# Kernel tuning notes

Hardware: AMD Instinct MI355X
Metric: run time of the kernel (lower is better)

The kernel has to match this reference:

```python
import jax, jax.numpy as jnp
import numpy as np

COMMITMENT_COST = 0.25


def setup_inputs() -> dict:
    key = jax.random.key(0)
    k1, k2 = jax.random.split(key)
    inputs = jax.random.normal(k1, (32, 64, 32, 32), dtype=jnp.float32)  # (B, C, H, W)
    embed = jax.random.normal(k2, (64, 1024), dtype=jnp.float32)          # (embedding_dim, num_embeddings)
    return {"inputs": inputs, "embed": embed}


def reference(inputs, embed):
    # Eval-mode forward (EMA buffer updates are training-only side effects).
    B, C, H, W = inputs.shape
    K = embed.shape[1]
    flat = inputs.transpose(0, 2, 3, 1).reshape(-1, C)  # (N, C)
    N = flat.shape[0]

    distances = (jnp.sum(flat * flat, axis=1, keepdims=True)
                 + jnp.sum(embed * embed, axis=0)
                 - 2.0 * flat @ embed)
    encoding_indices = jnp.argmin(distances, axis=1)  # (N,)

    # Gather instead of one-hot @ embed.T (same math, no N x K one-hot)
    quantized = embed.T[encoding_indices]  # (N, C)

    e_latent_loss = jnp.mean((jax.lax.stop_gradient(quantized) - flat) ** 2)
    loss = COMMITMENT_COST * e_latent_loss

    # straight-through estimator
    quantized_st = flat + jax.lax.stop_gradient(quantized - flat)
    quantized_out = quantized_st.reshape(B, H, W, C).transpose(0, 3, 1, 2)

    # avg_probs via scatter-add counts (== mean of one-hot encodings)
    counts = jnp.zeros((K,), dtype=flat.dtype).at[encoding_indices].add(1.0)
    avg_probs = counts / N
    perplexity = jnp.exp(-jnp.sum(avg_probs * jnp.log(avg_probs + 1e-10)))

    return quantized_out, loss, encoding_indices, perplexity
```

## Files before the change

kernel.cpp:

```cpp
#include <hip/hip_runtime.h>

#define N_PIX  32768
#define C_DIM  64
#define K_EMB  1024
#define HW     1024
#define P_TILE 8

#define OUT_Q_OFF    0
#define OUT_LOSS_OFF 2097152
#define OUT_IDX_OFF  2097153
#define OUT_PERP_OFF 2129921


__device__ __forceinline__ unsigned long long pack_score(float d, int k) {
    unsigned int u = __float_as_uint(d);
    u = (u & 0x80000000u) ? ~u : (u | 0x80000000u);
    return ((unsigned long long)u << 32) | (unsigned int)k;
}

__global__ __launch_bounds__(256, 4) void k_main(
    const float* __restrict__ inp, const float* __restrict__ embed,
    unsigned int* __restrict__ counts, float* __restrict__ lossAcc,
    float* __restrict__ out_q, float* __restrict__ out_idx) {
    __shared__ float x_lds[C_DIM * P_TILE];
    __shared__ unsigned long long red[4][P_TILE];
    __shared__ int ksel[P_TILE];
    __shared__ float lred[2];

    const int tid = threadIdx.x;
    const int n0  = blockIdx.x * P_TILE;
    const int b   = n0 >> 10;
    const int hw0 = n0 & 1023;
    const float* __restrict__ xu = inp + b * (C_DIM * HW) + hw0;

    if (tid < 128) {
        const int c  = tid >> 1;
        const int p4 = (tid & 1) * 4;
        *reinterpret_cast<float4*>(&x_lds[c * P_TILE + p4]) =
            *reinterpret_cast<const float4*>(xu + c * HW + p4);
    }
    __syncthreads();

    const int k0 = tid * 4;
    const float4* __restrict__ eb =
        reinterpret_cast<const float4*>(embed) + (k0 >> 2);

    float4 a0 = {0,0,0,0}, a1 = {0,0,0,0}, a2 = {0,0,0,0}, a3 = {0,0,0,0};
    float4 a4 = {0,0,0,0}, a5 = {0,0,0,0}, a6 = {0,0,0,0}, a7 = {0,0,0,0};
    float4 ee = {0,0,0,0};

#define FMA_P(i, xv, E) \
    a##i.x = fmaf((xv), E.x, a##i.x); \
    a##i.y = fmaf((xv), E.y, a##i.y); \
    a##i.z = fmaf((xv), E.z, a##i.z); \
    a##i.w = fmaf((xv), E.w, a##i.w);

#define BODY(E, c) { \
    const float4 xq0 = *reinterpret_cast<const float4*>(&x_lds[(c) * P_TILE + 0]); \
    const float4 xq1 = *reinterpret_cast<const float4*>(&x_lds[(c) * P_TILE + 4]); \
    ee.x = fmaf(E.x, E.x, ee.x); ee.y = fmaf(E.y, E.y, ee.y); \
    ee.z = fmaf(E.z, E.z, ee.z); ee.w = fmaf(E.w, E.w, ee.w); \
    FMA_P(0, xq0.x, E) FMA_P(1, xq0.y, E) FMA_P(2, xq0.z, E) FMA_P(3, xq0.w, E) \
    FMA_P(4, xq1.x, E) FMA_P(5, xq1.y, E) FMA_P(6, xq1.z, E) FMA_P(7, xq1.w, E) }

    float4 E0 = eb[0 * 256], E1 = eb[1 * 256], E2 = eb[2 * 256], E3 = eb[3 * 256];
#pragma unroll 1
    for (int c = 0; c < C_DIM; c += 4) {
        const int cn = (c + 4 < C_DIM) ? (c + 4) : c;
        float4 N0 = eb[(cn + 0) * 256];
        float4 N1 = eb[(cn + 1) * 256];
        float4 N2 = eb[(cn + 2) * 256];
        float4 N3 = eb[(cn + 3) * 256];
        BODY(E0, c + 0)
        BODY(E1, c + 1)
        BODY(E2, c + 2)
        BODY(E3, c + 3)
        E0 = N0; E1 = N1; E2 = N2; E3 = N3;
    }
#undef BODY
#undef FMA_P

    const int wv = tid >> 6, ln = tid & 63;
#define RED_P(i) { \
        const float s0 = fmaf(-2.f, a##i.x, ee.x); \
        const float s1 = fmaf(-2.f, a##i.y, ee.y); \
        const float s2 = fmaf(-2.f, a##i.z, ee.z); \
        const float s3 = fmaf(-2.f, a##i.w, ee.w); \
        unsigned long long m = pack_score(s0, k0), t; \
        t = pack_score(s1, k0 + 1); if (t < m) m = t; \
        t = pack_score(s2, k0 + 2); if (t < m) m = t; \
        t = pack_score(s3, k0 + 3); if (t < m) m = t; \
        for (int off = 32; off > 0; off >>= 1) { \
            unsigned long long o = __shfl_down(m, off, 64); \
            if (o < m) m = o; \
        } \
        if (ln == 0) red[wv][i] = m; }
    RED_P(0) RED_P(1) RED_P(2) RED_P(3)
    RED_P(4) RED_P(5) RED_P(6) RED_P(7)
#undef RED_P

    __syncthreads();
    if (tid < P_TILE) {
        unsigned long long m = red[0][tid];
        if (red[1][tid] < m) m = red[1][tid];
        if (red[2][tid] < m) m = red[2][tid];
        if (red[3][tid] < m) m = red[3][tid];
        const int k = (int)(unsigned int)(m & 0xFFFFFFFFull);
        ksel[tid] = k;
        out_idx[n0 + tid] = (float)k;
        atomicAdd(counts + k, 1u);
    }
    __syncthreads();

    if (tid < 128) {
        const int c  = tid >> 1;
        const int pb = (tid & 1) * 4;
        float ls = 0.f;
        float4 qv;
        float* qvp = &qv.x;
#pragma unroll
        for (int j = 0; j < 4; ++j) {
            const int k = ksel[pb + j];
            const float q  = embed[c * K_EMB + k];
            const float xv = x_lds[c * P_TILE + pb + j];
            const float d  = q - xv;
            ls = fmaf(d, d, ls);
            qvp[j] = q;
        }
        *reinterpret_cast<float4*>(out_q + b * (C_DIM * HW) + c * HW + hw0 + pb) = qv;
        for (int off = 32; off > 0; off >>= 1) ls += __shfl_down(ls, off, 64);
        if (ln == 0) lred[wv] = ls;
    }
    __syncthreads();
    if (tid == 0) atomicAdd(lossAcc, lred[0] + lred[1]);
}

__global__ __launch_bounds__(1024) void k_scalar(
    const unsigned int* __restrict__ counts, const float* __restrict__ lossAcc,
    float* __restrict__ out_loss, float* __restrict__ out_perp) {
    __shared__ float red[16];
    const int tid = threadIdx.x;
    float p = (float)counts[tid] * (1.0f / (float)N_PIX);
    float t = p * logf(p + 1e-10f);
    for (int off = 32; off > 0; off >>= 1) t += __shfl_down(t, off, 64);
    if ((tid & 63) == 0) red[tid >> 6] = t;
    __syncthreads();
    if (tid == 0) {
        float s = 0.f;
#pragma unroll
        for (int i = 0; i < 16; ++i) s += red[i];
        *out_perp = expf(-s);
        *out_loss = 0.25f * (*lossAcc) * (1.0f / (float)(N_PIX * C_DIM));
    }
}

extern "C" void kernel_launch(void* const* d_in, const int* in_sizes, int n_in,
                              void* d_out, int out_size, void* d_ws, size_t ws_size,
                              hipStream_t stream) {
    const float* inp   = (const float*)d_in[0];
    const float* embed = (const float*)d_in[1];
    float* out = (float*)d_out;

    char* ws = (char*)d_ws;
    unsigned int* counts  = (unsigned int*)(ws + 0);
    float*        lossAcc = (float*)(ws + 4096);

    hipMemsetAsync(ws, 0, 4096 + 16, stream);

    k_main<<<dim3(N_PIX / P_TILE), dim3(256), 0, stream>>>(
        inp, embed, counts, lossAcc, out + OUT_Q_OFF, out + OUT_IDX_OFF);
    k_scalar<<<dim3(1), dim3(1024), 0, stream>>>(counts, lossAcc,
        out + OUT_LOSS_OFF, out + OUT_PERP_OFF);
}
```

Baseline: 144.6 us.

## Compute distances with split-bf16 MFMA and exact fp32 top-2 rescoring

Replaces the scalar fp32 FMA distance loop with bf16 MFMA 32x32x16 instructions. Both the codebook and the inputs are split into three bf16 parts to approximate fp32 precision. A prep kernel precomputes the split codebook and the codebook norms, and the main kernel processes 64 pixels per block while tracking the top-2 candidates per pixel. The two candidates are rescored in exact fp32 so the argmin stays correct. The loss is computed algebraically from ||x||^2 plus the best distance, and the memset is replaced by zeroing device globals in the prep kernel. This trades some extra prep work, precision risk from the reduced-term split, and lower occupancy for much higher matrix throughput.

```diff
diff --git a/kernel.cpp b/kernel.cpp
--- a/kernel.cpp
+++ b/kernel.cpp
@@ -4,145 +4,257 @@
 #define C_DIM  64
 #define K_EMB  1024
 #define HW     1024
-#define P_TILE 8
+#define PIXB   64
 
 #define OUT_Q_OFF    0
 #define OUT_LOSS_OFF 2097152
 #define OUT_IDX_OFF  2097153
 #define OUT_PERP_OFF 2129921
 
-
+typedef __attribute__((ext_vector_type(8)))  __bf16 bf16x8;
+typedef __attribute__((ext_vector_type(16))) float  f32x16;
+
+__device__ unsigned short g_esplit[3 * K_EMB * C_DIM];
+__device__ float          g_ee[K_EMB];
+__device__ unsigned int   g_counts[K_EMB];
+__device__ float          g_lossAcc;
+
+__device__ __forceinline__ unsigned short f2bf(float f) {
+    unsigned u = __float_as_uint(f);
+    unsigned r = u + 0x7FFFu + ((u >> 16) & 1u);
+    return (unsigned short)(r >> 16);
+}
+__device__ __forceinline__ float bf2f(unsigned short b) {
+    return __uint_as_float(((unsigned)b) << 16);
+}
 __device__ __forceinline__ unsigned long long pack_score(float d, int k) {
     unsigned int u = __float_as_uint(d);
     u = (u & 0x80000000u) ? ~u : (u | 0x80000000u);
     return ((unsigned long long)u << 32) | (unsigned int)k;
 }
-
-__global__ __launch_bounds__(256, 4) void k_main(
+__device__ __forceinline__ uint4 pack8(const unsigned short* v) {
+    uint4 u;
+    u.x = (unsigned)v[0] | ((unsigned)v[1] << 16);
+    u.y = (unsigned)v[2] | ((unsigned)v[3] << 16);
+    u.z = (unsigned)v[4] | ((unsigned)v[5] << 16);
+    u.w = (unsigned)v[6] | ((unsigned)v[7] << 16);
+    return u;
+}
+__device__ __forceinline__ unsigned long long shfl_xor32_u64(unsigned long long v) {
+    unsigned lo = (unsigned)v, hi = (unsigned)(v >> 32);
+    lo = __shfl_xor(lo, 32, 64);
+    hi = __shfl_xor(hi, 32, 64);
+    return ((unsigned long long)hi << 32) | lo;
+}
+#define UPD2(P1, P2, MM) { \
+    if ((MM) < P1) { P2 = P1; P1 = (MM); } else if ((MM) < P2) P2 = (MM); }
+#define MRG2(P1, P2, O1, O2) { \
+    unsigned long long _lo = (O1) < P1 ? (O1) : P1; \
+    unsigned long long _hi = (O1) < P1 ? P1 : (O1); \
+    unsigned long long _m2 = (O2) < P2 ? (O2) : P2; \
+    P1 = _lo; P2 = _hi < _m2 ? _hi : _m2; }
+
+__global__ void k_prep(const float* __restrict__ embed) {
+    const int code = blockIdx.x * 64 + threadIdx.x;
+    if (code == 0) g_lossAcc = 0.f;
+    g_counts[code] = 0u;
+    const int tile = code >> 5, c32 = code & 31;
+    float ee = 0.f;
+#pragma unroll 8
+    for (int c = 0; c < C_DIM; ++c) {
+        const float x = embed[c * K_EMB + code];
+        ee = fmaf(x, x, ee);
+        const unsigned short b1 = f2bf(x);
+        const float r1 = x - bf2f(b1);
+        const unsigned short b2 = f2bf(r1);
+        const float r2 = r1 - bf2f(b2);
+        const unsigned short b3 = f2bf(r2);
+        const int s = c >> 4, hh = (c >> 3) & 1, e = c & 7;
+        const int rest = ((((tile * 4 + s) * 2 + hh) * 32) + c32) * 8 + e;
+        g_esplit[rest          ] = b1;
+        g_esplit[rest +  65536 ] = b2;
+        g_esplit[rest + 131072 ] = b3;
+    }
+    g_ee[code] = ee;
+}
+
+__global__ __launch_bounds__(256, 2) void k_main(
     const float* __restrict__ inp, const float* __restrict__ embed,
-    unsigned int* __restrict__ counts, float* __restrict__ lossAcc,
     float* __restrict__ out_q, float* __restrict__ out_idx) {
-    __shared__ float x_lds[C_DIM * P_TILE];
-    __shared__ unsigned long long red[4][P_TILE];
-    __shared__ int ksel[P_TILE];
-    __shared__ float lred[2];
+
+    __shared__ float x_raw[C_DIM * PIXB];
+    __shared__ uint4 xfrag[3 * 4 * 2 * PIXB];
+    __shared__ unsigned long long red1[4][PIXB];
+    __shared__ unsigned long long red2[4][PIXB];
+    __shared__ int   ksel[PIXB];
+    __shared__ float lred[4];
+    __shared__ float bdist;
 
     const int tid = threadIdx.x;
-    const int n0  = blockIdx.x * P_TILE;
+    const int n0  = blockIdx.x * PIXB;
     const int b   = n0 >> 10;
     const int hw0 = n0 & 1023;
-    const float* __restrict__ xu = inp + b * (C_DIM * HW) + hw0;
-
-    if (tid < 128) {
-        const int c  = tid >> 1;
-        const int p4 = (tid & 1) * 4;
-        *reinterpret_cast<float4*>(&x_lds[c * P_TILE + p4]) =
-            *reinterpret_cast<const float4*>(xu + c * HW + p4);
-    }
-    __syncthreads();
-
-    const int k0 = tid * 4;
-    const float4* __restrict__ eb =
-        reinterpret_cast<const float4*>(embed) + (k0 >> 2);
-
-    float4 a0 = {0,0,0,0}, a1 = {0,0,0,0}, a2 = {0,0,0,0}, a3 = {0,0,0,0};
-    float4 a4 = {0,0,0,0}, a5 = {0,0,0,0}, a6 = {0,0,0,0}, a7 = {0,0,0,0};
-    float4 ee = {0,0,0,0};
-
-#define FMA_P(i, xv, E) \
-    a##i.x = fmaf((xv), E.x, a##i.x); \
-    a##i.y = fmaf((xv), E.y, a##i.y); \
-    a##i.z = fmaf((xv), E.z, a##i.z); \
-    a##i.w = fmaf((xv), E.w, a##i.w);
-
-#define BODY(E, c) { \
-    const float4 xq0 = *reinterpret_cast<const float4*>(&x_lds[(c) * P_TILE + 0]); \
-    const float4 xq1 = *reinterpret_cast<const float4*>(&x_lds[(c) * P_TILE + 4]); \
-    ee.x = fmaf(E.x, E.x, ee.x); ee.y = fmaf(E.y, E.y, ee.y); \
-    ee.z = fmaf(E.z, E.z, ee.z); ee.w = fmaf(E.w, E.w, ee.w); \
-    FMA_P(0, xq0.x, E) FMA_P(1, xq0.y, E) FMA_P(2, xq0.z, E) FMA_P(3, xq0.w, E) \
-    FMA_P(4, xq1.x, E) FMA_P(5, xq1.y, E) FMA_P(6, xq1.z, E) FMA_P(7, xq1.w, E) }
-
-    float4 E0 = eb[0 * 256], E1 = eb[1 * 256], E2 = eb[2 * 256], E3 = eb[3 * 256];
+    const float* __restrict__ xg = inp + b * (C_DIM * HW) + hw0;
+
+#pragma unroll
+    for (int i = 0; i < 4; ++i) {
+        const int F = tid + i * 256;
+        const int c = F >> 4, p4 = (F & 15) << 2;
+        *reinterpret_cast<float4*>(&x_raw[F << 2]) =
+            *reinterpret_cast<const float4*>(xg + c * HW + p4);
+    }
+    __syncthreads();
+
+    float sx2 = 0.f;
+#pragma unroll
+    for (int cc = 0; cc < 2; ++cc) {
+        const int cid = tid + cc * 256;
+        const int s = cid >> 7, hh = (cid >> 6) & 1, p = cid & 63;
+        unsigned short b1[8], b2[8], b3[8];
+#pragma unroll
+        for (int e = 0; e < 8; ++e) {
+            const float x = x_raw[(s * 16 + hh * 8 + e) * PIXB + p];
+            sx2 = fmaf(x, x, sx2);
+            b1[e] = f2bf(x);
+            const float r1 = x - bf2f(b1[e]);
+            b2[e] = f2bf(r1);
+            const float r2 = r1 - bf2f(b2[e]);
+            b3[e] = f2bf(r2);
+        }
+        const int fi = (s * 2 + hh) * PIXB + p;
+        xfrag[fi            ] = pack8(b1);
+        xfrag[fi + 8 * PIXB ] = pack8(b2);
+        xfrag[fi + 16 * PIXB] = pack8(b3);
+    }
+    for (int off = 32; off; off >>= 1) sx2 += __shfl_down(sx2, off, 64);
+    if ((tid & 63) == 0) lred[tid >> 6] = sx2;
+    __syncthreads();
+
+    const int w   = tid >> 6;
+    const int ln  = tid & 63;
+    const int c31 = ln & 31;
+    const int h   = ln >> 5;
+    const uint4* __restrict__ eg = reinterpret_cast<const uint4*>(g_esplit);
+
+    unsigned long long p1a = ~0ull, p2a = ~0ull;
+    unsigned long long p1b = ~0ull, p2b = ~0ull;
+
 #pragma unroll 1
-    for (int c = 0; c < C_DIM; c += 4) {
-        const int cn = (c + 4 < C_DIM) ? (c + 4) : c;
-        float4 N0 = eb[(cn + 0) * 256];
-        float4 N1 = eb[(cn + 1) * 256];
-        float4 N2 = eb[(cn + 2) * 256];
-        float4 N3 = eb[(cn + 3) * 256];
-        BODY(E0, c + 0)
-        BODY(E1, c + 1)
-        BODY(E2, c + 2)
-        BODY(E3, c + 3)
-        E0 = N0; E1 = N1; E2 = N2; E3 = N3;
-    }
-#undef BODY
-#undef FMA_P
-
-    const int wv = tid >> 6, ln = tid & 63;
-#define RED_P(i) { \
-        const float s0 = fmaf(-2.f, a##i.x, ee.x); \
-        const float s1 = fmaf(-2.f, a##i.y, ee.y); \
-        const float s2 = fmaf(-2.f, a##i.z, ee.z); \
-        const float s3 = fmaf(-2.f, a##i.w, ee.w); \
-        unsigned long long m = pack_score(s0, k0), t; \
-        t = pack_score(s1, k0 + 1); if (t < m) m = t; \
-        t = pack_score(s2, k0 + 2); if (t < m) m = t; \
-        t = pack_score(s3, k0 + 3); if (t < m) m = t; \
-        for (int off = 32; off > 0; off >>= 1) { \
-            unsigned long long o = __shfl_down(m, off, 64); \
-            if (o < m) m = o; \
-        } \
-        if (ln == 0) red[wv][i] = m; }
-    RED_P(0) RED_P(1) RED_P(2) RED_P(3)
-    RED_P(4) RED_P(5) RED_P(6) RED_P(7)
-#undef RED_P
-
-    __syncthreads();
-    if (tid < P_TILE) {
-        unsigned long long m = red[0][tid];
-        if (red[1][tid] < m) m = red[1][tid];
-        if (red[2][tid] < m) m = red[2][tid];
-        if (red[3][tid] < m) m = red[3][tid];
+    for (int r = 0; r < 8; ++r) {
+        const int ct = r * 4 + w;
+        const int cb = ct * 32;
+
+        uint4 ae[3][4];
+#pragma unroll
+        for (int j = 0; j < 3; ++j)
+#pragma unroll
+            for (int s = 0; s < 4; ++s)
+                ae[j][s] = eg[(((j * 32 + ct) * 4 + s) * 2 + h) * 32 + c31];
+
+        float eev[16];
+#pragma unroll
+        for (int rg = 0; rg < 16; ++rg)
+            eev[rg] = g_ee[cb + (rg & 3) + 8 * (rg >> 2) + 4 * h];
+
+#pragma unroll
+        for (int pt = 0; pt < 2; ++pt) {
+            const int pbase = pt * 32 + c31;
+            f32x16 acc = {};
+#pragma unroll
+            for (int ib = 0; ib < 3; ++ib) {
+                uint4 bx[4];
+#pragma unroll
+                for (int s = 0; s < 4; ++s)
+                    bx[s] = xfrag[(ib * 8 + s * 2 + h) * PIXB + pbase];
+#pragma unroll
+                for (int ja = 0; ja < 3 - ib; ++ja)
+#pragma unroll
+                    for (int s = 0; s < 4; ++s)
+                        acc = __builtin_amdgcn_mfma_f32_32x32x16_bf16(
+                            __builtin_bit_cast(bf16x8, ae[ja][s]),
+                            __builtin_bit_cast(bf16x8, bx[s]),
+                            acc, 0, 0, 0);
+            }
+#pragma unroll
+            for (int rg = 0; rg < 16; ++rg) {
+                const float dist = fmaf(-2.f, acc[rg], eev[rg]);
+                const unsigned long long mm =
+                    pack_score(dist, cb + (rg & 3) + 8 * (rg >> 2) + 4 * h);
+                if (pt == 0) { UPD2(p1a, p2a, mm) }
+                else         { UPD2(p1b, p2b, mm) }
+            }
+        }
+    }
+
+    {
+        unsigned long long o1 = shfl_xor32_u64(p1a), o2 = shfl_xor32_u64(p2a);
+        MRG2(p1a, p2a, o1, o2)
+        o1 = shfl_xor32_u64(p1b); o2 = shfl_xor32_u64(p2b);
+        MRG2(p1b, p2b, o1, o2)
+        if (ln < 32) {
+            red1[w][ln] = p1a; red2[w][ln] = p2a;
+            red1[w][ln + 32] = p1b; red2[w][ln + 32] = p2b;
+        }
+    }
+    __syncthreads();
+
+    if (tid < PIXB) {
+        unsigned long long M1 = red1[0][tid], M2 = red2[0][tid];
+        MRG2(M1, M2, red1[1][tid], red2[1][tid])
+        MRG2(M1, M2, red1[2][tid], red2[2][tid])
+        MRG2(M1, M2, red1[3][tid], red2[3][tid])
+        const int k1 = (int)(unsigned int)(M1 & 0xFFFFFFFFull);
+        const int k2 = (int)(unsigned int)(M2 & 0xFFFFFFFFull);
+        float d1 = 0.f, d2 = 0.f;
+        const float* xcol = x_raw + tid;
+#pragma unroll 8
+        for (int c = 0; c < C_DIM; ++c) {
+            const float xv = xcol[c * PIXB];
+            d1 = fmaf(xv, embed[c * K_EMB + k1], d1);
+            d2 = fmaf(xv, embed[c * K_EMB + k2], d2);
+        }
+        const float dist1 = fmaf(-2.f, d1, g_ee[k1]);
+        const float dist2 = fmaf(-2.f, d2, g_ee[k2]);
+        const unsigned long long s1 = pack_score(dist1, k1);
+        const unsigned long long s2 = pack_score(dist2, k2);
+        const unsigned long long m = s1 < s2 ? s1 : s2;
         const int k = (int)(unsigned int)(m & 0xFFFFFFFFull);
         ksel[tid] = k;
         out_idx[n0 + tid] = (float)k;
-        atomicAdd(counts + k, 1u);
-    }
-    __syncthreads();
-
-    if (tid < 128) {
-        const int c  = tid >> 1;
-        const int pb = (tid & 1) * 4;
-        float ls = 0.f;
-        float4 qv;
-        float* qvp = &qv.x;
-#pragma unroll
-        for (int j = 0; j < 4; ++j) {
-            const int k = ksel[pb + j];
-            const float q  = embed[c * K_EMB + k];
-            const float xv = x_lds[c * P_TILE + pb + j];
-            const float d  = q - xv;
-            ls = fmaf(d, d, ls);
-            qvp[j] = q;
-        }
-        *reinterpret_cast<float4*>(out_q + b * (C_DIM * HW) + c * HW + hw0 + pb) = qv;
-        for (int off = 32; off > 0; off >>= 1) ls += __shfl_down(ls, off, 64);
-        if (ln == 0) lred[wv] = ls;
-    }
-    __syncthreads();
-    if (tid == 0) atomicAdd(lossAcc, lred[0] + lred[1]);
-}
-
-__global__ __launch_bounds__(1024) void k_scalar(
-    const unsigned int* __restrict__ counts, const float* __restrict__ lossAcc,
-    float* __restrict__ out_loss, float* __restrict__ out_perp) {
+        atomicAdd(g_counts + k, 1u);
+        const unsigned int u = (unsigned int)(m >> 32);
+        float dist = __uint_as_float((u & 0x80000000u) ? (u & 0x7FFFFFFFu) : ~u);
+        for (int off = 32; off; off >>= 1) dist += __shfl_down(dist, off, 64);
+        if (tid == 0) bdist = dist;
+    }
+    __syncthreads();
+
+    {
+        const int c  = tid >> 2;
+        const int p0 = (tid & 3) * 16;
+        float* oq = out_q + b * (C_DIM * HW) + c * HW + hw0 + p0;
+        const float* er = embed + c * K_EMB;
+#pragma unroll
+        for (int i = 0; i < 4; ++i) {
+            float4 q;
+            q.x = er[ksel[p0 + i * 4 + 0]];
+            q.y = er[ksel[p0 + i * 4 + 1]];
+            q.z = er[ksel[p0 + i * 4 + 2]];
+            q.w = er[ksel[p0 + i * 4 + 3]];
+            *reinterpret_cast<float4*>(oq + i * 4) = q;
+        }
+    }
+    if (tid == 0)
+        atomicAdd(&g_lossAcc, lred[0] + lred[1] + lred[2] + lred[3] + bdist);
+}
+
+__global__ __launch_bounds__(1024) void k_scalar(float* __restrict__ out_loss,
+                                                 float* __restrict__ out_perp) {
     __shared__ float red[16];
     const int tid = threadIdx.x;
-    float p = (float)counts[tid] * (1.0f / (float)N_PIX);
+    float p = (float)g_counts[tid] * (1.0f / (float)N_PIX);
     float t = p * logf(p + 1e-10f);
-    for (int off = 32; off > 0; off >>= 1) t += __shfl_down(t, off, 64);
+    for (int off = 32; off; off >>= 1) t += __shfl_down(t, off, 64);
     if ((tid & 63) == 0) red[tid >> 6] = t;
     __syncthreads();
     if (tid == 0) {
@@ -150,7 +262,7 @@
 #pragma unroll
         for (int i = 0; i < 16; ++i) s += red[i];
         *out_perp = expf(-s);
-        *out_loss = 0.25f * (*lossAcc) * (1.0f / (float)(N_PIX * C_DIM));
+        *out_loss = 0.25f * g_lossAcc * (1.0f / (float)(N_PIX * C_DIM));
     }
 }
 
@@ -161,14 +273,9 @@
     const float* embed = (const float*)d_in[1];
     float* out = (float*)d_out;
 
-    char* ws = (char*)d_ws;
-    unsigned int* counts  = (unsigned int*)(ws + 0);
-    float*        lossAcc = (float*)(ws + 4096);
-
-    hipMemsetAsync(ws, 0, 4096 + 16, stream);
-
-    k_main<<<dim3(N_PIX / P_TILE), dim3(256), 0, stream>>>(
-        inp, embed, counts, lossAcc, out + OUT_Q_OFF, out + OUT_IDX_OFF);
-    k_scalar<<<dim3(1), dim3(1024), 0, stream>>>(counts, lossAcc,
-        out + OUT_LOSS_OFF, out + OUT_PERP_OFF);
-}
+    k_prep<<<dim3(16), dim3(64), 0, stream>>>(embed);
+    k_main<<<dim3(N_PIX / PIXB), dim3(256), 0, stream>>>(
+        inp, embed, out + OUT_Q_OFF, out + OUT_IDX_OFF);
+    k_scalar<<<dim3(1), dim3(1024), 0, stream>>>(out + OUT_LOSS_OFF,
+                                                 out + OUT_PERP_OFF);
+}
```

After: 117.0 us. -19.1%, faster.
